# Kernel tuning notes

Hardware: AMD Instinct MI355X
Metric: run time of the kernel (lower is better)

## Reference

```python
import jax, jax.numpy as jnp
import numpy as np

N_EL = 1024
N_UP = 512
D_EMB = 256
WIDTH = 64

def get_all_pair_indices(n_el, n_up):
    # static numpy precompute, identical to the source module
    ii, jj = np.meshgrid(np.arange(n_el), np.arange(n_el), indexing='ij')
    spin = np.concatenate([np.zeros(n_up, dtype=int), np.ones(n_el - n_up, dtype=int)])
    idx = np.stack([ii.flatten(), jj.flatten()], axis=0)
    idx = idx[:, idx[0] != idx[1]]
    same = spin[idx[0]] == spin[idx[1]]
    return idx[:, same], idx[:, ~same]

_PAIRS = get_all_pair_indices(N_EL, N_UP)

def logscaled_diff_features(diff):
    # [P,3] diff -> [P,4]: log-rescaled diff vector + log1p(distance)
    r = jnp.linalg.norm(diff, axis=-1, keepdims=True)
    return jnp.concatenate([diff * jnp.log1p(r) / r, jnp.log1p(r)], axis=-1)

def mlp3(x, W0, b0, W1, b1, W2, b2=None):
    h = jnp.tanh(x @ W0 + b0)
    h = jnp.tanh(h @ W1 + b1)
    out = h @ W2
    return out if b2 is None else out + b2

def _forward(electrons, embeddings, A_same, A_diff, Ws0_same, bs0_same, Ws1_same, bs1_same, Ws2_same, Ws0_diff, bs0_diff, Ws1_diff, bs1_diff, Ws2_diff, scale_same, scale_diff, We0, be0, We1, be1, We2, be2, mlp_scale, log_bias):
    (ics, ins_), (icd, ind_) = _PAIRS
    diff_same = electrons[ics] - electrons[ins_]   # [P_same,3]
    diff_diff = electrons[icd] - electrons[ind_]   # [P_diff,3]
    dist_same = jnp.linalg.norm(diff_same, axis=-1)
    dist_diff = jnp.linalg.norm(diff_diff, axis=-1)
    # Yukawa e-e cusp
    A_s = jax.nn.softplus(A_same); F_s = jnp.sqrt(2 * A_s)
    A_d = jax.nn.softplus(A_diff); F_d = jnp.sqrt(2 * A_d)
    logpsi = A_s * jnp.sum(jnp.expm1(-dist_same / F_s) / dist_same)
    logpsi = logpsi + A_d * jnp.sum(jnp.expm1(-dist_diff / F_d) / dist_diff)
    # pairwise e-e MLPs
    fs = logscaled_diff_features(diff_same)
    fd = logscaled_diff_features(diff_diff)
    logpsi = logpsi + jnp.sum(mlp3(fs, Ws0_same, bs0_same, Ws1_same, bs1_same, Ws2_same)) * scale_same
    logpsi = logpsi + jnp.sum(mlp3(fd, Ws0_diff, bs0_diff, Ws1_diff, bs1_diff, Ws2_diff)) * scale_diff
    # per-electron embedding MLP jastrow
    J = mlp3(embeddings, We0, be0, We1, be1, We2, be2) * mlp_scale  # [n_el, 2]
    J = J + jnp.stack([jnp.zeros(()), log_bias])
    jastrows = J.sum(axis=0)  # (2,)
    log_J = jastrows[1]
    sign = jnp.sign(log_J)
    logpsi = logpsi + jastrows[0] + jnp.log(jnp.abs(log_J))
    return sign, logpsi

def setup_inputs():
    key = jax.random.key(0)
    ks = jax.random.split(key, 16)
    rn = lambda k, s: jax.random.normal(k, s, dtype=jnp.float32)
    return dict(
        electrons=rn(ks[0], (N_EL, 3)),
        embeddings=rn(ks[1], (N_EL, D_EMB)),
        A_same=jnp.ones(()), A_diff=jnp.ones(()),
        Ws0_same=rn(ks[2], (4, WIDTH)) * 0.3, bs0_same=jnp.zeros((WIDTH,)),
        Ws1_same=rn(ks[3], (WIDTH, WIDTH)) * 0.1, bs1_same=jnp.zeros((WIDTH,)),
        Ws2_same=rn(ks[4], (WIDTH, 1)) * 0.1,
        Ws0_diff=rn(ks[5], (4, WIDTH)) * 0.3, bs0_diff=jnp.zeros((WIDTH,)),
        Ws1_diff=rn(ks[6], (WIDTH, WIDTH)) * 0.1, bs1_diff=jnp.zeros((WIDTH,)),
        Ws2_diff=rn(ks[7], (WIDTH, 1)) * 0.1,
        scale_same=rn(ks[8], ()) * 0.1, scale_diff=rn(ks[9], ()) * 0.1,
        We0=rn(ks[10], (D_EMB, WIDTH)) * 0.05, be0=jnp.zeros((WIDTH,)),
        We1=rn(ks[11], (WIDTH, WIDTH)) * 0.1, be1=jnp.zeros((WIDTH,)),
        We2=rn(ks[12], (WIDTH, 2)) * 0.1, be2=jnp.zeros((2,)),
        mlp_scale=rn(ks[13], (2,)) * 0.1,
        log_bias=jnp.ones(()),
    )

def reference(electrons, embeddings, A_same, A_diff, Ws0_same, bs0_same, Ws1_same, bs1_same, Ws2_same, Ws0_diff, bs0_diff, Ws1_diff, bs1_diff, Ws2_diff, scale_same, scale_diff, We0, be0, We1, be1, We2, be2, mlp_scale, log_bias):
    return _forward(electrons, embeddings, A_same, A_diff, Ws0_same, bs0_same, Ws1_same, bs1_same, Ws2_same, Ws0_diff, bs0_diff, Ws1_diff, bs1_diff, Ws2_diff, scale_same, scale_diff, We0, be0, We1, be1, We2, be2, mlp_scale, log_bias)
```

## Files before the change

### kernel.cpp

```cpp
#include <hip/hip_runtime.h>
#include <hip/hip_bf16.h>

#define NEL 1024
#define NUP 512
#define DEMB 256
#define WID 64

typedef __attribute__((ext_vector_type(8))) short bf16x8;
typedef __attribute__((ext_vector_type(4))) float f32x4;
typedef __attribute__((ext_vector_type(16))) float f32x16;

#define CTANH 2.8853900817779268f
#define LOG2E 1.4426950408889634f
#define LN2   0.6931471805599453f


__device__ __forceinline__ float tanh_pre(float y) {
    float e = __builtin_amdgcn_exp2f(y);
    return fmaf(-2.0f, __builtin_amdgcn_rcpf(e + 1.0f), 1.0f);
}

__device__ __forceinline__ short f2bf(float x) {
    unsigned u = __builtin_bit_cast(unsigned, x);
    u += 0x7FFFu + ((u >> 16) & 1u);
    return (short)(u >> 16);
}

__device__ __forceinline__ float softplus_f(float x) {
    return fmaxf(x, 0.0f) + __logf(1.0f + __expf(-fabsf(x)));
}

__global__ __launch_bounds__(256) void prep_kernel(
    const float* __restrict__ W0s, const float* __restrict__ b0s,
    const float* __restrict__ W1s, const float* __restrict__ b1s, const float* __restrict__ W2s,
    const float* __restrict__ W0d, const float* __restrict__ b0d,
    const float* __restrict__ W1d, const float* __restrict__ b1d, const float* __restrict__ W2d,
    const float* __restrict__ As, const float* __restrict__ Ad,
    const float* __restrict__ ss, const float* __restrict__ sd,
    float* __restrict__ wsf)
{
    short* w1ws = (short*)(wsf + 4096);
    const int b = blockIdx.x, tid = threadIdx.x;
    if (b < 16) {
        const int s = b >> 3, c = b & 7;
        const float* W1 = s ? W1d : W1s;
        #pragma unroll
        for (int it = 0; it < 2; ++it) {
            const int local = (c << 9) + (it << 8) + tid;
            const int n = local >> 6, k = local & 63;
            w1ws[s * 4608 + n * 72 + k] = f2bf(CTANH * W1[k * 64 + n]);
        }
    } else {
        for (int idx = tid; idx < 2048; idx += 256) wsf[idx] = 0.0f;
        #pragma unroll
        for (int s = 0; s < 2; ++s) {
            const float* W0 = s ? W0d : W0s;
            const float* b0 = s ? b0d : b0s;
            const float* b1 = s ? b1d : b1s;
            const float* w2 = s ? W2d : W2s;
            const float scl = (s ? sd : ss)[0];
            const int base = 2048 + s * 1024;
            { const int k = tid >> 6, n = tid & 63; wsf[base + n * 4 + k] = CTANH * W0[tid]; }
            if (tid < 64) {
                wsf[base + 256 + tid] = CTANH * b0[tid];
                wsf[base + 320 + tid] = CTANH * b1[tid];
                wsf[base + 384 + tid] = scl * w2[tid];
            }
            if (tid == 0) {
                const float A = softplus_f((s ? Ad : As)[0]);
                wsf[base + 448] = A;
                wsf[base + 449] = LOG2E * __builtin_amdgcn_rsqf(2.0f * A);
            }
        }
    }
}

__global__ __launch_bounds__(256, 2) void pair_kernel(
    const float* __restrict__ electrons,
    const float* __restrict__ wsf,
    float* __restrict__ accum)
{
    __shared__ __align__(16) short w1t[4608];
    __shared__ __align__(16) float w0t[256];
    __shared__ float b0sh[64], b1sh[64], w2sh[64];
    __shared__ float wsum[4];

    const int tid  = threadIdx.x;
    const int bidx = blockIdx.x;
    const int i  = bidx >> 3;
    const int jb = (bidx & 7) << 7;
    const int sset = ((i < NUP) == (jb < NUP)) ? 0 : 1;
    const float* wbase = wsf + 2048 + sset * 1024;
    const short* w1g   = (const short*)(wsf + 4096) + sset * 4608;

    {
        const float4* src = (const float4*)w1g;
        float4* dst = (float4*)w1t;
        for (int idx = tid; idx < 576; idx += 256) dst[idx] = src[idx];
        if (tid < 64) {
            ((float4*)w0t)[tid] = ((const float4*)wbase)[tid];
            b0sh[tid] = wbase[256 + tid];
            b1sh[tid] = wbase[320 + tid];
            w2sh[tid] = wbase[384 + tid];
        }
    }
    const float A     = wbase[448];
    const float invF2 = wbase[449];
    __syncthreads();

    const int lane = tid & 63, wv = tid >> 6;
    const int hi = lane >> 5, p32 = lane & 31;
    const int j = jb + (wv << 5) + p32;
    const bool diag = (j == i);

    const float eix = electrons[3 * i], eiy = electrons[3 * i + 1], eiz = electrons[3 * i + 2];
    float dx = eix - electrons[3 * j];
    float dy = eiy - electrons[3 * j + 1];
    float dz = eiz - electrons[3 * j + 2];
    if (diag) { dx = 0.0f; dy = 0.0f; dz = 0.0f; }
    float r2 = fmaf(dx, dx, fmaf(dy, dy, dz * dz));
    if (diag) r2 = 1.0f;
    const float rr    = __builtin_amdgcn_sqrtf(r2);
    const float inv_r = __builtin_amdgcn_rcpf(rr);
    const float l1p   = __builtin_amdgcn_logf(1.0f + rr) * LN2;
    const float gf    = l1p * inv_r;
    const float f0 = dx * gf, f1 = dy * gf, f2v = dz * gf;
    const float f3 = diag ? 0.0f : l1p;
    const float cusp = (hi == 0 && !diag)
        ? A * (__builtin_amdgcn_exp2f(-rr * invF2) - 1.0f) * inv_r : 0.0f;

    bf16x8 afr[4];
    #pragma unroll
    for (int kc = 0; kc < 4; ++kc) {
        #pragma unroll
        for (int e = 0; e < 8; ++e) {
            const int n = (kc << 4) + (hi << 3) + e;
            f32x4 w = *(const f32x4*)&w0t[n << 2];
            float y = fmaf(f3, w[3], fmaf(f2v, w[2], fmaf(f1, w[1], fmaf(f0, w[0], b0sh[n]))));
            afr[kc][e] = __bfloat16_as_ushort(__float2bfloat16(tanh_pre(y)));
        }
    }

    f32x16 acc0, acc1;
    #pragma unroll
    for (int q = 0; q < 4; ++q) {
        const f32x4 v0 = *(const f32x4*)&b1sh[(q << 3) + (hi << 2)];
        const f32x4 v1 = *(const f32x4*)&b1sh[32 + (q << 3) + (hi << 2)];
        #pragma unroll
        for (int e = 0; e < 4; ++e) { acc0[(q << 2) + e] = v0[e]; acc1[(q << 2) + e] = v1[e]; }
    }
    const short* w1r0 = &w1t[p32 * 72 + (hi << 3)];
    const short* w1r1 = &w1t[(32 + p32) * 72 + (hi << 3)];
    #pragma unroll
    for (int kc = 0; kc < 4; ++kc) {
        bf16x8 wa0 = *(const bf16x8*)(w1r0 + (kc << 4));
        bf16x8 wa1 = *(const bf16x8*)(w1r1 + (kc << 4));
        acc0 = __builtin_amdgcn_mfma_f32_32x32x16_bf16(wa0, afr[kc], acc0, 0, 0, 0);
        acc1 = __builtin_amdgcn_mfma_f32_32x32x16_bf16(wa1, afr[kc], acc1, 0, 0, 0);
    }

    float s = 0.0f;
    #pragma unroll
    for (int q = 0; q < 4; ++q) {
        const f32x4 u0 = *(const f32x4*)&w2sh[(q << 3) + (hi << 2)];
        const f32x4 u1 = *(const f32x4*)&w2sh[32 + (q << 3) + (hi << 2)];
        #pragma unroll
        for (int e = 0; e < 4; ++e) {
            s = fmaf(tanh_pre(acc0[(q << 2) + e]), u0[e], s);
            s = fmaf(tanh_pre(acc1[(q << 2) + e]), u1[e], s);
        }
    }
    if (diag) s = 0.0f;
    float partial = s + cusp;

    #pragma unroll
    for (int off = 32; off; off >>= 1) partial += __shfl_down(partial, off);
    if (lane == 0) wsum[wv] = partial;
    __syncthreads();
    if (tid == 0)
        atomicAdd(&accum[(bidx & 63) << 4], wsum[0] + wsum[1] + wsum[2] + wsum[3]);
}

__global__ __launch_bounds__(256) void embed_kernel(
    const float* __restrict__ emb,
    const float* __restrict__ We0, const float* __restrict__ be0,
    const float* __restrict__ We1, const float* __restrict__ be1,
    const float* __restrict__ We2, const float* __restrict__ be2,
    const float* __restrict__ mlp_scale, const float* __restrict__ log_bias,
    float* __restrict__ accum)
{
    __shared__ float xs[DEMB];
    __shared__ float part1[4 * WID];
    __shared__ float h0s[WID];
    __shared__ float part2[4 * WID];
    const int tid = threadIdx.x, wv = tid >> 6, lane = tid & 63;
    const int r = blockIdx.x;

    xs[tid] = emb[(r << 8) + tid];
    __syncthreads();

    const int kb = wv << 6;
    float a0 = 0, a1 = 0, a2 = 0, a3 = 0;
    #pragma unroll
    for (int q = 0; q < 64; q += 4) {
        a0 = fmaf(xs[kb + q],     We0[(kb + q)     * WID + lane], a0);
        a1 = fmaf(xs[kb + q + 1], We0[(kb + q + 1) * WID + lane], a1);
        a2 = fmaf(xs[kb + q + 2], We0[(kb + q + 2) * WID + lane], a2);
        a3 = fmaf(xs[kb + q + 3], We0[(kb + q + 3) * WID + lane], a3);
    }
    part1[(wv << 6) + lane] = (a0 + a1) + (a2 + a3);
    __syncthreads();

    if (wv == 0) {
        const float s = part1[lane] + part1[64 + lane] + part1[128 + lane]
                      + part1[192 + lane] + be0[lane];
        h0s[lane] = tanh_pre(CTANH * s);
    }
    __syncthreads();

    const int kb2 = wv << 4;
    float c0 = 0, c1 = 0;
    #pragma unroll
    for (int q = 0; q < 16; q += 2) {
        c0 = fmaf(h0s[kb2 + q],     We1[(kb2 + q)     * WID + lane], c0);
        c1 = fmaf(h0s[kb2 + q + 1], We1[(kb2 + q + 1) * WID + lane], c1);
    }
    part2[(wv << 6) + lane] = c0 + c1;
    __syncthreads();

    if (wv == 0) {
        const float c = part2[lane] + part2[64 + lane] + part2[128 + lane]
                      + part2[192 + lane] + be1[lane];
        const float h1 = tanh_pre(CTANH * c);
        float p0 = h1 * We2[2 * lane], p1 = h1 * We2[2 * lane + 1];
        #pragma unroll
        for (int off = 32; off; off >>= 1) {
            p0 += __shfl_down(p0, off);
            p1 += __shfl_down(p1, off);
        }
        if (lane == 0) {
            const int b = (r & 63) << 4;
            atomicAdd(&accum[1024 + b], (p0 + be2[0]) * mlp_scale[0]);
            atomicAdd(&accum[1032 + b], (p1 + be2[1]) * mlp_scale[1] + log_bias[0]);
        }
    }
}

__global__ __launch_bounds__(64) void final_kernel(const float* __restrict__ accum,
                                                   float* __restrict__ out)
{
    const int lane = threadIdx.x;
    float v  = accum[lane << 4];
    float j0 = accum[1024 + (lane << 4)];
    float j1 = accum[1032 + (lane << 4)];
    #pragma unroll
    for (int off = 32; off; off >>= 1) {
        v  += __shfl_down(v, off);
        j0 += __shfl_down(j0, off);
        j1 += __shfl_down(j1, off);
    }
    if (lane == 0) {
        const float sign = (j1 > 0.0f) ? 1.0f : ((j1 < 0.0f) ? -1.0f : 0.0f);
        out[0] = sign;
        out[1] = v + j0 + logf(fabsf(j1));
    }
}

extern "C" void kernel_launch(void* const* d_in, const int* in_sizes, int n_in,
                              void* d_out, int out_size, void* d_ws, size_t ws_size,
                              hipStream_t stream) {
    const float* electrons  = (const float*)d_in[0];
    const float* embeddings = (const float*)d_in[1];
    const float* A_same     = (const float*)d_in[2];
    const float* A_diff     = (const float*)d_in[3];
    const float* Ws0_same   = (const float*)d_in[4];
    const float* bs0_same   = (const float*)d_in[5];
    const float* Ws1_same   = (const float*)d_in[6];
    const float* bs1_same   = (const float*)d_in[7];
    const float* Ws2_same   = (const float*)d_in[8];
    const float* Ws0_diff   = (const float*)d_in[9];
    const float* bs0_diff   = (const float*)d_in[10];
    const float* Ws1_diff   = (const float*)d_in[11];
    const float* bs1_diff   = (const float*)d_in[12];
    const float* Ws2_diff   = (const float*)d_in[13];
    const float* scale_same = (const float*)d_in[14];
    const float* scale_diff = (const float*)d_in[15];
    const float* We0        = (const float*)d_in[16];
    const float* be0        = (const float*)d_in[17];
    const float* We1        = (const float*)d_in[18];
    const float* be1        = (const float*)d_in[19];
    const float* We2        = (const float*)d_in[20];
    const float* be2        = (const float*)d_in[21];
    const float* mlp_scale  = (const float*)d_in[22];
    const float* log_bias   = (const float*)d_in[23];

    float* out = (float*)d_out;
    float* wsf = (float*)d_ws;

    hipLaunchKernelGGL(prep_kernel, dim3(17), dim3(256), 0, stream,
        Ws0_same, bs0_same, Ws1_same, bs1_same, Ws2_same,
        Ws0_diff, bs0_diff, Ws1_diff, bs1_diff, Ws2_diff,
        A_same, A_diff, scale_same, scale_diff, wsf);

    hipLaunchKernelGGL(pair_kernel, dim3(NEL * NEL / 128), dim3(256), 0, stream,
        electrons, wsf, wsf);

    hipLaunchKernelGGL(embed_kernel, dim3(NEL), dim3(256), 0, stream,
        embeddings, We0, be0, We1, be1, We2, be2, mlp_scale, log_bias, wsf);

    hipLaunchKernelGGL(final_kernel, dim3(1), dim3(64), 0, stream, wsf, out);
}
```

Measured before the change: 52.09 us.

## Switch pair MLP to packed fp16 math with polynomial tanh and fp16 MFMA

Replaces the fp32 first-layer evaluation and exp/rcp-based tanh with packed half2 arithmetic and a clamped odd polynomial tanh approximation. The second layer now runs on fp16 MFMA using weights pre-swizzled into fragment order, so they are copied to LDS and read without padding. Occupancy is raised via launch bounds, LDS use is smaller, and the accumulator layout is compacted. The aim is to cut transcendental and VALU cost per pair, at the cost of fp16 precision and a tanh approximation that clamps at ±4, which may hurt accuracy.

```diff
diff --git a/kernel.cpp b/kernel.cpp
--- a/kernel.cpp
+++ b/kernel.cpp
@@ -1,14 +1,15 @@
 #include <hip/hip_runtime.h>
-#include <hip/hip_bf16.h>
 
 #define NEL 1024
 #define NUP 512
 #define DEMB 256
 #define WID 64
 
-typedef __attribute__((ext_vector_type(8))) short bf16x8;
 typedef __attribute__((ext_vector_type(4))) float f32x4;
 typedef __attribute__((ext_vector_type(16))) float f32x16;
+typedef __attribute__((ext_vector_type(4))) unsigned int u32x4;
+typedef __attribute__((ext_vector_type(8))) _Float16 f16x8;
+typedef __attribute__((ext_vector_type(2))) _Float16 h2;
 
 #define CTANH 2.8853900817779268f
 #define LOG2E 1.4426950408889634f
@@ -20,14 +21,27 @@
     return fmaf(-2.0f, __builtin_amdgcn_rcpf(e + 1.0f), 1.0f);
 }
 
-__device__ __forceinline__ short f2bf(float x) {
-    unsigned u = __builtin_bit_cast(unsigned, x);
-    u += 0x7FFFu + ((u >> 16) & 1u);
-    return (short)(u >> 16);
-}
-
 __device__ __forceinline__ float softplus_f(float x) {
     return fmaxf(x, 0.0f) + __logf(1.0f + __expf(-fabsf(x)));
+}
+
+__device__ __forceinline__ h2 h2s(float f) {
+    _Float16 v = (_Float16)f; h2 r; r[0] = v; r[1] = v; return r;
+}
+__device__ __forceinline__ h2 bch2(unsigned u) { return __builtin_bit_cast(h2, u); }
+__device__ __forceinline__ unsigned h2bits(h2 h) { return __builtin_bit_cast(unsigned, h); }
+
+__device__ __forceinline__ h2 tanh2(h2 x) {
+    x = __builtin_elementwise_min(h2s(4.0f), __builtin_elementwise_max(h2s(-4.0f), x));
+    h2 xq = x * h2s(0.25f);
+    h2 v  = xq * xq;
+    h2 p  = h2s(-5.150581f);
+    p = p * v + h2s(16.252870f);
+    p = p * v + h2s(-19.909140f);
+    p = p * v + h2s(12.125338f);
+    p = p * v + h2s(-4.052176f);
+    p = p * v + h2s(0.983638f);
+    return x * p;
 }
 
 __global__ __launch_bounds__(256) void prep_kernel(
@@ -39,19 +53,21 @@
     const float* __restrict__ ss, const float* __restrict__ sd,
     float* __restrict__ wsf)
 {
-    short* w1ws = (short*)(wsf + 4096);
     const int b = blockIdx.x, tid = threadIdx.x;
     if (b < 16) {
-        const int s = b >> 3, c = b & 7;
+        const int s = b >> 3, h = (b >> 2) & 1, kc = b & 3;
         const float* W1 = s ? W1d : W1s;
+        _Float16* w1out = (_Float16*)(wsf + 2048) + s * 4096 + (h * 4 + kc) * 512;
         #pragma unroll
         for (int it = 0; it < 2; ++it) {
-            const int local = (c << 9) + (it << 8) + tid;
-            const int n = local >> 6, k = local & 63;
-            w1ws[s * 4608 + n * 72 + k] = f2bf(CTANH * W1[k * 64 + n]);
+            const int id = tid + it * 256;
+            const int l = id >> 3, e = id & 7;
+            const int k = kc * 16 + (l >> 5) * 8 + e;
+            const int n = h * 32 + (l & 31);
+            w1out[id] = (_Float16)W1[k * 64 + n];
         }
     } else {
-        for (int idx = tid; idx < 2048; idx += 256) wsf[idx] = 0.0f;
+        for (int idx = tid; idx < 1024; idx += 256) wsf[idx] = 0.0f;
         #pragma unroll
         for (int s = 0; s < 2; ++s) {
             const float* W0 = s ? W0d : W0s;
@@ -59,54 +75,60 @@
             const float* b1 = s ? b1d : b1s;
             const float* w2 = s ? W2d : W2s;
             const float scl = (s ? sd : ss)[0];
-            const int base = 2048 + s * 1024;
-            { const int k = tid >> 6, n = tid & 63; wsf[base + n * 4 + k] = CTANH * W0[tid]; }
+            const int base = 1024 + s * 512;
+            if (tid < 64) wsf[base + tid] = b1[tid];
             if (tid < 64) {
-                wsf[base + 256 + tid] = CTANH * b0[tid];
-                wsf[base + 320 + tid] = CTANH * b1[tid];
-                wsf[base + 384 + tid] = scl * w2[tid];
+                const int h = tid >> 5, hi = (tid >> 4) & 1, rp = (tid >> 1) & 7, wh = tid & 1;
+                const int n = h * 32 + ((2 * rp) & 3) + 8 * (rp >> 1) + 4 * hi + wh;
+                ((_Float16*)(wsf + base + 64))[tid] = (_Float16)(scl * w2[n]);
+            }
+            {
+                const int kc = tid >> 6, hi = (tid >> 5) & 1, ep = (tid >> 3) & 3;
+                const int k = (tid >> 1) & 3, wh = tid & 1;
+                const int n = kc * 16 + hi * 8 + 2 * ep + wh;
+                ((_Float16*)(wsf + base + 96))[tid] = (_Float16)W0[k * 64 + n];
+            }
+            if (tid < 64) {
+                const int kc = tid >> 4, hi = (tid >> 3) & 1, ep = (tid >> 1) & 3, wh = tid & 1;
+                ((_Float16*)(wsf + base + 224))[tid] = (_Float16)b0[kc * 16 + hi * 8 + 2 * ep + wh];
             }
             if (tid == 0) {
                 const float A = softplus_f((s ? Ad : As)[0]);
-                wsf[base + 448] = A;
-                wsf[base + 449] = LOG2E * __builtin_amdgcn_rsqf(2.0f * A);
+                wsf[base + 256] = A;
+                wsf[base + 257] = LOG2E * __builtin_amdgcn_rsqf(2.0f * A);
             }
         }
     }
 }
 
-__global__ __launch_bounds__(256, 2) void pair_kernel(
+__global__ __launch_bounds__(256, 6) void pair_kernel(
     const float* __restrict__ electrons,
     const float* __restrict__ wsf,
     float* __restrict__ accum)
 {
-    __shared__ __align__(16) short w1t[4608];
-    __shared__ __align__(16) float w0t[256];
-    __shared__ float b0sh[64], b1sh[64], w2sh[64];
-    __shared__ float wsum[4];
+    __shared__ __align__(16) char smem[8592];
+    char*  w1lds = smem;
+    float* b1sh  = (float*)(smem + 8192);
+    char*  w2lds = smem + 8448;
+    float* wsum  = (float*)(smem + 8576);
 
     const int tid  = threadIdx.x;
     const int bidx = blockIdx.x;
     const int i  = bidx >> 3;
     const int jb = (bidx & 7) << 7;
     const int sset = ((i < NUP) == (jb < NUP)) ? 0 : 1;
-    const float* wbase = wsf + 2048 + sset * 1024;
-    const short* w1g   = (const short*)(wsf + 4096) + sset * 4608;
+    const float* tb = wsf + 1024 + sset * 512;
 
     {
-        const float4* src = (const float4*)w1g;
-        float4* dst = (float4*)w1t;
-        for (int idx = tid; idx < 576; idx += 256) dst[idx] = src[idx];
-        if (tid < 64) {
-            ((float4*)w0t)[tid] = ((const float4*)wbase)[tid];
-            b0sh[tid] = wbase[256 + tid];
-            b1sh[tid] = wbase[320 + tid];
-            w2sh[tid] = wbase[384 + tid];
-        }
-    }
-    const float A     = wbase[448];
-    const float invF2 = wbase[449];
-    __syncthreads();
+        const float4* src = (const float4*)(wsf + 2048 + sset * 2048);
+        float4* dst = (float4*)w1lds;
+        dst[tid]       = src[tid];
+        dst[tid + 256] = src[tid + 256];
+        if (tid < 16) ((float4*)b1sh)[tid] = ((const float4*)tb)[tid];
+        if (tid < 8)  ((float4*)w2lds)[tid] = ((const float4*)(tb + 64))[tid];
+    }
+    const float A     = tb[256];
+    const float invF2 = tb[257];
 
     const int lane = tid & 63, wv = tid >> 6;
     const int hi = lane >> 5, p32 = lane & 31;
@@ -124,54 +146,70 @@
     const float inv_r = __builtin_amdgcn_rcpf(rr);
     const float l1p   = __builtin_amdgcn_logf(1.0f + rr) * LN2;
     const float gf    = l1p * inv_r;
-    const float f0 = dx * gf, f1 = dy * gf, f2v = dz * gf;
-    const float f3 = diag ? 0.0f : l1p;
     const float cusp = (hi == 0 && !diag)
         ? A * (__builtin_amdgcn_exp2f(-rr * invF2) - 1.0f) * inv_r : 0.0f;
 
-    bf16x8 afr[4];
+    const h2 fs0 = h2s(dx * gf);
+    const h2 fs1 = h2s(dy * gf);
+    const h2 fs2 = h2s(dz * gf);
+    const h2 fs3 = h2s(diag ? 0.0f : l1p);
+
+    __syncthreads();
+
+    const char* w0g = (const char*)(tb + 96);
+    const char* b0g = (const char*)(tb + 224);
+    f16x8 afr[4];
     #pragma unroll
     for (int kc = 0; kc < 4; ++kc) {
-        #pragma unroll
-        for (int e = 0; e < 8; ++e) {
-            const int n = (kc << 4) + (hi << 3) + e;
-            f32x4 w = *(const f32x4*)&w0t[n << 2];
-            float y = fmaf(f3, w[3], fmaf(f2v, w[2], fmaf(f1, w[1], fmaf(f0, w[0], b0sh[n]))));
-            afr[kc][e] = __bfloat16_as_ushort(__float2bfloat16(tanh_pre(y)));
-        }
-    }
-
-    f32x16 acc0, acc1;
-    #pragma unroll
-    for (int q = 0; q < 4; ++q) {
-        const f32x4 v0 = *(const f32x4*)&b1sh[(q << 3) + (hi << 2)];
-        const f32x4 v1 = *(const f32x4*)&b1sh[32 + (q << 3) + (hi << 2)];
-        #pragma unroll
-        for (int e = 0; e < 4; ++e) { acc0[(q << 2) + e] = v0[e]; acc1[(q << 2) + e] = v1[e]; }
-    }
-    const short* w1r0 = &w1t[p32 * 72 + (hi << 3)];
-    const short* w1r1 = &w1t[(32 + p32) * 72 + (hi << 3)];
-    #pragma unroll
-    for (int kc = 0; kc < 4; ++kc) {
-        bf16x8 wa0 = *(const bf16x8*)(w1r0 + (kc << 4));
-        bf16x8 wa1 = *(const bf16x8*)(w1r1 + (kc << 4));
-        acc0 = __builtin_amdgcn_mfma_f32_32x32x16_bf16(wa0, afr[kc], acc0, 0, 0, 0);
-        acc1 = __builtin_amdgcn_mfma_f32_32x32x16_bf16(wa1, afr[kc], acc1, 0, 0, 0);
-    }
-
-    float s = 0.0f;
-    #pragma unroll
-    for (int q = 0; q < 4; ++q) {
-        const f32x4 u0 = *(const f32x4*)&w2sh[(q << 3) + (hi << 2)];
-        const f32x4 u1 = *(const f32x4*)&w2sh[32 + (q << 3) + (hi << 2)];
-        #pragma unroll
-        for (int e = 0; e < 4; ++e) {
-            s = fmaf(tanh_pre(acc0[(q << 2) + e]), u0[e], s);
-            s = fmaf(tanh_pre(acc1[(q << 2) + e]), u1[e], s);
-        }
-    }
-    if (diag) s = 0.0f;
-    float partial = s + cusp;
+        const u32x4 b0v = *(const u32x4*)(b0g + (((kc << 1) + hi) << 4));
+        u32x4 frag;
+        #pragma unroll
+        for (int ep = 0; ep < 4; ++ep) {
+            const u32x4 wv4 = *(const u32x4*)(w0g + (((kc << 1) + hi) << 6) + (ep << 4));
+            h2 a = bch2(b0v[ep]);
+            a = bch2(wv4[0]) * fs0 + a;
+            a = bch2(wv4[1]) * fs1 + a;
+            a = bch2(wv4[2]) * fs2 + a;
+            a = bch2(wv4[3]) * fs3 + a;
+            frag[ep] = h2bits(tanh2(a));
+        }
+        afr[kc] = __builtin_bit_cast(f16x8, frag);
+    }
+
+    float ssum = 0.0f;
+    #pragma unroll
+    for (int h = 0; h < 2; ++h) {
+        f32x16 acc;
+        #pragma unroll
+        for (int q = 0; q < 4; ++q) {
+            const f32x4 bv = *(const f32x4*)(b1sh + (h << 5) + (q << 3) + (hi << 2));
+            #pragma unroll
+            for (int e = 0; e < 4; ++e) acc[(q << 2) + e] = bv[e];
+        }
+        #pragma unroll
+        for (int kc = 0; kc < 4; ++kc) {
+            const f16x8 wa = *(const f16x8*)(w1lds + ((((h << 2) + kc) << 6) + lane) * 16);
+            acc = __builtin_amdgcn_mfma_f32_32x32x16_f16(wa, afr[kc], acc, 0, 0, 0);
+        }
+        const char* w2c = w2lds + (((h << 1) + hi) << 5);
+        const u32x4 w2a = *(const u32x4*)(w2c);
+        const u32x4 w2b = *(const u32x4*)(w2c + 16);
+        h2 s2 = h2s(0.0f);
+        #pragma unroll
+        for (int q = 0; q < 4; ++q) {
+            h2 p0; p0[0] = (_Float16)acc[(q << 2) + 0]; p0[1] = (_Float16)acc[(q << 2) + 1];
+            h2 p1; p1[0] = (_Float16)acc[(q << 2) + 2]; p1[1] = (_Float16)acc[(q << 2) + 3];
+            const h2 t0 = tanh2(p0);
+            const h2 t1 = tanh2(p1);
+            const unsigned wlo = (q < 2) ? w2a[(q << 1)]     : w2b[((q - 2) << 1)];
+            const unsigned whi = (q < 2) ? w2a[(q << 1) + 1] : w2b[((q - 2) << 1) + 1];
+            s2 = t0 * bch2(wlo) + s2;
+            s2 = t1 * bch2(whi) + s2;
+        }
+        ssum += (float)s2[0] + (float)s2[1];
+    }
+    if (diag) ssum = 0.0f;
+    float partial = ssum + cusp;
 
     #pragma unroll
     for (int off = 32; off; off >>= 1) partial += __shfl_down(partial, off);
@@ -240,8 +278,8 @@
         }
         if (lane == 0) {
             const int b = (r & 63) << 4;
-            atomicAdd(&accum[1024 + b], (p0 + be2[0]) * mlp_scale[0]);
-            atomicAdd(&accum[1032 + b], (p1 + be2[1]) * mlp_scale[1] + log_bias[0]);
+            atomicAdd(&accum[b + 4], (p0 + be2[0]) * mlp_scale[0]);
+            atomicAdd(&accum[b + 8], (p1 + be2[1]) * mlp_scale[1] + log_bias[0]);
         }
     }
 }
@@ -250,9 +288,9 @@
                                                    float* __restrict__ out)
 {
     const int lane = threadIdx.x;
-    float v  = accum[lane << 4];
-    float j0 = accum[1024 + (lane << 4)];
-    float j1 = accum[1032 + (lane << 4)];
+    float v  = accum[(lane << 4)];
+    float j0 = accum[(lane << 4) + 4];
+    float j1 = accum[(lane << 4) + 8];
     #pragma unroll
     for (int off = 32; off; off >>= 1) {
         v  += __shfl_down(v, off);
@@ -280,7 +318,7 @@
     const float* Ws2_same   = (const float*)d_in[8];
     const float* Ws0_diff   = (const float*)d_in[9];
     const float* bs0_diff   = (const float*)d_in[10];
-    const float* Ws1_diff   = (const float*)d_in[11];
+    const float* bs1w_diff  = (const float*)d_in[11];
     const float* bs1_diff   = (const float*)d_in[12];
     const float* Ws2_diff   = (const float*)d_in[13];
     const float* scale_same = (const float*)d_in[14];
@@ -299,7 +337,7 @@
 
     hipLaunchKernelGGL(prep_kernel, dim3(17), dim3(256), 0, stream,
         Ws0_same, bs0_same, Ws1_same, bs1_same, Ws2_same,
-        Ws0_diff, bs0_diff, Ws1_diff, bs1_diff, Ws2_diff,
+        Ws0_diff, bs0_diff, bs1w_diff, bs1_diff, Ws2_diff,
         A_same, A_diff, scale_same, scale_diff, wsf);
 
     hipLaunchKernelGGL(pair_kernel, dim3(NEL * NEL / 128), dim3(256), 0, stream,
```

New measurement: 49.87 us. -4.3%, faster.
